# Performance work log

Hardware: AMD Instinct MI355X
Metric: run time of the kernel (lower is better)

Reference implementation:

```python
import jax, jax.numpy as jnp
import numpy as np

N_NODES = 50000
N_EDGES = 800000
HEADS = 2
HID = 64
NEG_SLOPE = 0.2


def setup_inputs() -> dict:
    key = jax.random.key(0)
    ks = jax.random.split(key, 8)
    x = jax.random.normal(ks[0], (N_NODES, 128), dtype=jnp.float32)
    W_src = jax.random.normal(ks[1], (128, HEADS * HID), dtype=jnp.float32) * (1.0 / np.sqrt(128))
    W_dst = jax.random.normal(ks[2], (128, HEADS * HID), dtype=jnp.float32) * (1.0 / np.sqrt(128))
    att_src = jax.random.normal(ks[3], (HEADS, HID), dtype=jnp.float32) * 0.1
    att_dst = jax.random.normal(ks[4], (HEADS, HID), dtype=jnp.float32) * 0.1
    bias = jax.random.normal(ks[5], (HEADS * HID,), dtype=jnp.float32) * 0.01
    prelu_w = jnp.full((HEADS * HID,), 0.25, dtype=jnp.float32)
    edge_index = jax.random.randint(ks[6], (2, N_EDGES), 0, N_NODES, dtype=jnp.int64)
    return {"x": x, "W_src": W_src, "W_dst": W_dst, "att_src": att_src,
            "att_dst": att_dst, "bias": bias, "prelu_w": prelu_w,
            "edge_index": edge_index}


def gat_prelu(x, W_src, W_dst, att_src, att_dst, bias, prelu_w, edge_index):
    N = x.shape[0]
    src, dst = edge_index[0], edge_index[1]
    xs = (x @ W_src).reshape(N, HEADS, HID)   # [N,H,C]
    xd = (x @ W_dst).reshape(N, HEADS, HID)
    a_src = jnp.einsum('nhc,hc->nh', xs, att_src)  # [N,H]
    a_dst = jnp.einsum('nhc,hc->nh', xd, att_dst)
    e = jax.nn.leaky_relu(a_src[src] + a_dst[dst], NEG_SLOPE)  # [E,H]
    # segment softmax over incoming edges of each dst node
    m = jax.ops.segment_max(e, dst, num_segments=N)            # [N,H]
    ee = jnp.exp(e - m[dst])
    denom = jax.ops.segment_sum(ee, dst, num_segments=N)
    alpha = ee / (denom[dst] + 1e-16)                          # [E,H]
    msg = xs[src] * alpha[:, :, None]                          # [E,H,C]
    out = jax.ops.segment_sum(msg, dst, num_segments=N)        # [N,H,C]
    out = out.reshape(N, HEADS * HID) + bias
    return jnp.where(out >= 0, out, prelu_w * out)


def reference(x, W_src, W_dst, att_src, att_dst, bias, prelu_w, edge_index):
    return gat_prelu(x, W_src, W_dst, att_src, att_dst, bias, prelu_w, edge_index)
```

## Files before the change

### kernel.cpp

```cpp
#include <hip/hip_runtime.h>
#include <hip/hip_fp16.h>


#define N_NODES 50000
#define N_EDGES 800000
#define CAP     56

#define OFF_A    0
#define OFF_CNT  800000
#define OFF_XS   1000000
#define OFF_BKT  13800000
#define OFF_SWZ  36200000

typedef _Float16 f16x8 __attribute__((ext_vector_type(8)));
typedef float    f32x4 __attribute__((ext_vector_type(4)));

__global__ __launch_bounds__(256) void k0_prep(
    const float* __restrict__ Wsrc, const float* __restrict__ Wdst,
    const float* __restrict__ att_s, const float* __restrict__ att_d,
    __half* __restrict__ swz, int* __restrict__ cnt)
{
    __shared__ float vS[128 * 4];
    const int nt = blockIdx.x;
    const int t = threadIdx.x;
    for (int i = nt * 256 + t; i < N_NODES; i += 9 * 256) cnt[i] = 0;

    if (nt == 8) {
        if (t < 128) {
            const float* wsp = Wsrc + t * 128;
            const float* wdp = Wdst + t * 128;
            float a0 = 0.f, a1 = 0.f, a2 = 0.f, a3 = 0.f;
#pragma unroll 8
            for (int c = 0; c < 64; ++c) {
                a0 += wsp[c]      * att_s[c];
                a1 += wsp[64 + c] * att_s[64 + c];
                a2 += wdp[c]      * att_d[c];
                a3 += wdp[64 + c] * att_d[64 + c];
            }
            *(float4*)(vS + t * 4) = make_float4(a0, a1, a2, a3);
        }
        __syncthreads();
    }
    const int kb = t >> 6, L = t & 63;
    const int col = L & 15;
    const int krow = kb * 32 + ((L >> 4) & 3) * 8;
    f16x8 v;
    if (nt < 8) {
#pragma unroll
        for (int j = 0; j < 8; ++j)
            v[j] = (_Float16)Wsrc[(size_t)(krow + j) * 128 + nt * 16 + col];
    } else {
#pragma unroll
        for (int j = 0; j < 8; ++j)
            v[j] = (col < 4) ? (_Float16)vS[(krow + j) * 4 + col] : (_Float16)0.f;
    }
    *(f16x8*)(swz + ((size_t)(kb * 9 + nt) * 64 + L) * 8) = v;
}

__global__ __launch_bounds__(256) void k1_gemm(
    const float* __restrict__ x, const __half* __restrict__ swz,
    __half* __restrict__ xs, float* __restrict__ a_all)
{
    const int t = threadIdx.x;
    const int w = t >> 6, L = t & 63;
    const int m = L & 15, q = L >> 4;
    const int n_a = blockIdx.x * 64 + w * 16 + m;
    const int rrow = (n_a < N_NODES) ? n_a : (N_NODES - 1);
    const float* xrow = x + (size_t)rrow * 128;

    f32x4 acc[9];
#pragma unroll
    for (int nt = 0; nt < 9; ++nt) acc[nt] = (f32x4){0.f, 0.f, 0.f, 0.f};

#pragma unroll
    for (int kb = 0; kb < 4; ++kb) {
        const int k0 = kb * 32 + q * 8;
        float4 xa = *(const float4*)(xrow + k0);
        float4 xb = *(const float4*)(xrow + k0 + 4);
        f16x8 a;
        a[0] = (_Float16)xa.x; a[1] = (_Float16)xa.y;
        a[2] = (_Float16)xa.z; a[3] = (_Float16)xa.w;
        a[4] = (_Float16)xb.x; a[5] = (_Float16)xb.y;
        a[6] = (_Float16)xb.z; a[7] = (_Float16)xb.w;
        const f16x8* bbase = (const f16x8*)swz + (size_t)(kb * 9) * 64 + L;
#pragma unroll
        for (int nt = 0; nt < 9; ++nt) {
            f16x8 b = bbase[(size_t)nt * 64];
            acc[nt] = __builtin_amdgcn_mfma_f32_16x16x32_f16(a, b, acc[nt], 0, 0, 0);
        }
    }

    const int rbase = blockIdx.x * 64 + w * 16 + q * 4;
#pragma unroll
    for (int nt = 0; nt < 8; ++nt) {
#pragma unroll
        for (int r = 0; r < 4; ++r) {
            int n = rbase + r;
            if (n < N_NODES)
                xs[(size_t)n * 128 + nt * 16 + m] = (__half)acc[nt][r];
        }
    }
    if (m < 4) {
#pragma unroll
        for (int r = 0; r < 4; ++r) {
            int n = rbase + r;
            if (n < N_NODES) a_all[(size_t)n * 4 + m] = acc[8][r];
        }
    }
}

__global__ __launch_bounds__(256) void k5_scatter(
    const int* __restrict__ ei, const float* __restrict__ a_all,
    int* __restrict__ cnt, int2* __restrict__ bkt)
{
    int e = (blockIdx.x * 256 + threadIdx.x) * 2;
    if (e >= N_EDGES) return;
    int2 ss = *(const int2*)(ei + e);
    int2 dd = *(const int2*)(ei + N_EDGES + e);
    float4 as0 = *(const float4*)(a_all + (size_t)ss.x * 4);
    float4 ad0 = *(const float4*)(a_all + (size_t)dd.x * 4);
    float4 as1 = *(const float4*)(a_all + (size_t)ss.y * 4);
    float4 ad1 = *(const float4*)(a_all + (size_t)dd.y * 4);

    float e00 = as0.x + ad0.z, e01 = as0.y + ad0.w;
    float e10 = as1.x + ad1.z, e11 = as1.y + ad1.w;
    e00 = (e00 >= 0.f) ? e00 : 0.2f * e00;
    e01 = (e01 >= 0.f) ? e01 : 0.2f * e01;
    e10 = (e10 >= 0.f) ? e10 : 0.2f * e10;
    e11 = (e11 >= 0.f) ? e11 : 0.2f * e11;
    __half2 hw0 = __floats2half2_rn(__expf(e00), __expf(e01));
    __half2 hw1 = __floats2half2_rn(__expf(e10), __expf(e11));

    int pos0 = atomicAdd(cnt + dd.x, 1);
    int pos1 = atomicAdd(cnt + dd.y, 1);
    if (pos0 < CAP) {
        int2 ent; ent.x = ss.x; ent.y = *reinterpret_cast<int*>(&hw0);
        bkt[(size_t)dd.x * CAP + pos0] = ent;
    }
    if (pos1 < CAP) {
        int2 ent; ent.x = ss.y; ent.y = *reinterpret_cast<int*>(&hw1);
        bkt[(size_t)dd.y * CAP + pos1] = ent;
    }
}

template<bool GUARD>
__device__ __forceinline__ void step8(const int2* __restrict__ row, int k, int m,
                                      int sh, int j, const __half* __restrict__ xs,
                                      float& ax, float& ay, float& sw)
{
    int4 p0 = *(const int4*)(row + k);
    int4 p1 = *(const int4*)(row + k + 2);
    int4 p2 = *(const int4*)(row + k + 4);
    int4 p3 = *(const int4*)(row + k + 6);
    int s0 = p0.x, s1 = p0.z, s2 = p1.x, s3 = p1.z;
    int s4 = p2.x, s5 = p2.z, s6 = p3.x, s7 = p3.z;
    unsigned w0 = (unsigned)p0.y, w1 = (unsigned)p0.w;
    unsigned w2 = (unsigned)p1.y, w3 = (unsigned)p1.w;
    unsigned w4 = (unsigned)p2.y, w5 = (unsigned)p2.w;
    unsigned w6 = (unsigned)p3.y, w7 = (unsigned)p3.w;
    if (GUARD) {
        if (k + 0 >= m) { s0 = 0; w0 = 0; }
        if (k + 1 >= m) { s1 = 0; w1 = 0; }
        if (k + 2 >= m) { s2 = 0; w2 = 0; }
        if (k + 3 >= m) { s3 = 0; w3 = 0; }
        if (k + 4 >= m) { s4 = 0; w4 = 0; }
        if (k + 5 >= m) { s5 = 0; w5 = 0; }
        if (k + 6 >= m) { s6 = 0; w6 = 0; }
        if (k + 7 >= m) { s7 = 0; w7 = 0; }
    }
    __half2 h0 = *(const __half2*)(xs + (size_t)s0 * 128 + j);
    __half2 h1 = *(const __half2*)(xs + (size_t)s1 * 128 + j);
    __half2 h2 = *(const __half2*)(xs + (size_t)s2 * 128 + j);
    __half2 h3 = *(const __half2*)(xs + (size_t)s3 * 128 + j);
    __half2 h4 = *(const __half2*)(xs + (size_t)s4 * 128 + j);
    __half2 h5 = *(const __half2*)(xs + (size_t)s5 * 128 + j);
    __half2 h6 = *(const __half2*)(xs + (size_t)s6 * 128 + j);
    __half2 h7 = *(const __half2*)(xs + (size_t)s7 * 128 + j);
    float a0 = __half2float(__ushort_as_half((unsigned short)(w0 >> sh)));
    float a1 = __half2float(__ushort_as_half((unsigned short)(w1 >> sh)));
    float a2 = __half2float(__ushort_as_half((unsigned short)(w2 >> sh)));
    float a3 = __half2float(__ushort_as_half((unsigned short)(w3 >> sh)));
    float a4 = __half2float(__ushort_as_half((unsigned short)(w4 >> sh)));
    float a5 = __half2float(__ushort_as_half((unsigned short)(w5 >> sh)));
    float a6 = __half2float(__ushort_as_half((unsigned short)(w6 >> sh)));
    float a7 = __half2float(__ushort_as_half((unsigned short)(w7 >> sh)));
    ax += __half2float(h0.x) * a0; ay += __half2float(h0.y) * a0;
    ax += __half2float(h1.x) * a1; ay += __half2float(h1.y) * a1;
    ax += __half2float(h2.x) * a2; ay += __half2float(h2.y) * a2;
    ax += __half2float(h3.x) * a3; ay += __half2float(h3.y) * a3;
    ax += __half2float(h4.x) * a4; ay += __half2float(h4.y) * a4;
    ax += __half2float(h5.x) * a5; ay += __half2float(h5.y) * a5;
    ax += __half2float(h6.x) * a6; ay += __half2float(h6.y) * a6;
    ax += __half2float(h7.x) * a7; ay += __half2float(h7.y) * a7;
    sw += ((a0 + a1) + (a2 + a3)) + ((a4 + a5) + (a6 + a7));
}

__global__ __launch_bounds__(256) void k6_agg(
    const int2* __restrict__ bkt, const int* __restrict__ cnt,
    const __half* __restrict__ xs, const float* __restrict__ bias,
    const float* __restrict__ prelu_w, float* __restrict__ out)
{
    const int n = blockIdx.x * 4 + (threadIdx.x >> 6);
    const int lane = threadIdx.x & 63;
    const int j = lane * 2;
    const int sh = (lane >> 5) * 16;
    int m = cnt[n]; if (m > CAP) m = CAP;
    const int2* row = bkt + (size_t)n * CAP;
    float ax = 0.f, ay = 0.f, sw = 0.f;
    int k = 0;
    for (; k + 8 <= m; k += 8)
        step8<false>(row, k, m, sh, j, xs, ax, ay, sw);
    if (k < m)
        step8<true>(row, k, m, sh, j, xs, ax, ay, sw);

    float inv = 1.f / (sw + 1e-16f);
    float o0 = ax * inv + bias[j];
    float o1 = ay * inv + bias[j + 1];
    float2 r;
    r.x = (o0 >= 0.f) ? o0 : prelu_w[j] * o0;
    r.y = (o1 >= 0.f) ? o1 : prelu_w[j + 1] * o1;
    *(float2*)(out + (size_t)n * 128 + j) = r;
}

extern "C" void kernel_launch(void* const* d_in, const int* in_sizes, int n_in,
                              void* d_out, int out_size, void* d_ws, size_t ws_size,
                              hipStream_t stream) {
    const float* x      = (const float*)d_in[0];
    const float* Wsrc   = (const float*)d_in[1];
    const float* Wdst   = (const float*)d_in[2];
    const float* att_s  = (const float*)d_in[3];
    const float* att_d  = (const float*)d_in[4];
    const float* bias   = (const float*)d_in[5];
    const float* prelu  = (const float*)d_in[6];
    const int*   ei     = (const int*)d_in[7];
    float* out = (float*)d_out;

    char* ws = (char*)d_ws;
    float*  a_all = (float*)(ws + OFF_A);
    int*    cnt   = (int*)(ws + OFF_CNT);
    __half* xs    = (__half*)(ws + OFF_XS);
    int2*   bkt   = (int2*)(ws + OFF_BKT);
    __half* swz   = (__half*)(ws + OFF_SWZ);

    k0_prep<<<9, 256, 0, stream>>>(Wsrc, Wdst, att_s, att_d, swz, cnt);
    k1_gemm<<<(N_NODES + 63) / 64, 256, 0, stream>>>(x, swz, xs, a_all);
    k5_scatter<<<(N_EDGES / 2 + 255) / 256, 256, 0, stream>>>(ei, a_all, cnt, bkt);
    k6_agg<<<N_NODES / 4, 256, 0, stream>>>(bkt, cnt, xs, bias, prelu, out);
}
```

Baseline: 193.8 us.

## Replace direct edge scatter with two-pass coarse/fine bucketed binning

Replaces the single scatter kernel, which did random global atomics and writes per edge, with two passes. First, edges are binned by the coarse destination range (1024 nodes) into per-block shared-memory rings and flushed in 8-entry chunks to coarse buckets, with the source and low destination bits packed into one 64-bit entry. Second, each coarse bucket is read sequentially and scattered into the per-node CAP buckets, so the atomics and writes land in a localized range. This adds a kernel launch and extra traffic, and uses the output buffer as scratch. Coarse buckets are capped at BCAP with no overflow handling, and the 16-bit source packing cannot hold indices of 65536 or more.

```diff
diff --git a/kernel.cpp b/kernel.cpp
--- a/kernel.cpp
+++ b/kernel.cpp
@@ -5,25 +5,31 @@
 #define N_NODES 50000
 #define N_EDGES 800000
 #define CAP     56
-
-#define OFF_A    0
-#define OFF_CNT  800000
-#define OFF_XS   1000000
-#define OFF_BKT  13800000
-#define OFF_SWZ  36200000
+#define NB      49
+#define BCAP    20480
+#define RING    64
+
+#define OFF_A      0
+#define OFF_CNT    800000
+#define OFF_GCUR   1000000
+#define OFF_XS     1000256
+#define OFF_BKT    13800256
+#define OFF_SWZ    36200256
 
 typedef _Float16 f16x8 __attribute__((ext_vector_type(8)));
 typedef float    f32x4 __attribute__((ext_vector_type(4)));
+typedef unsigned long long u64;
 
 __global__ __launch_bounds__(256) void k0_prep(
     const float* __restrict__ Wsrc, const float* __restrict__ Wdst,
     const float* __restrict__ att_s, const float* __restrict__ att_d,
-    __half* __restrict__ swz, int* __restrict__ cnt)
+    __half* __restrict__ swz, int* __restrict__ cnt, int* __restrict__ gcur)
 {
     __shared__ float vS[128 * 4];
     const int nt = blockIdx.x;
     const int t = threadIdx.x;
     for (int i = nt * 256 + t; i < N_NODES; i += 9 * 256) cnt[i] = 0;
+    if (nt == 0 && t < NB) gcur[t] = t * BCAP;
 
     if (nt == 8) {
         if (t < 128) {
@@ -109,37 +115,87 @@
     }
 }
 
-__global__ __launch_bounds__(256) void k5_scatter(
+__global__ __launch_bounds__(256) void kC_coarse(
     const int* __restrict__ ei, const float* __restrict__ a_all,
+    int* __restrict__ gcur, u64* __restrict__ coarse)
+{
+    __shared__ u64 ring[NB * RING];
+    __shared__ int lcnt[NB], ltail[NB];
+    const int t = threadIdx.x;
+    if (t < NB) { lcnt[t] = 0; ltail[t] = 0; }
+    __syncthreads();
+
+    const int per = gridDim.x * 512;
+    const int nIter = (N_EDGES + per - 1) / per;
+    for (int it = 0; it < nIter; ++it) {
+        const int base = it * per + blockIdx.x * 512;
+#pragma unroll
+        for (int u = 0; u < 2; ++u) {
+            int e = base + u * 256 + t;
+            if (e < N_EDGES) {
+                int s = ei[e];
+                int d = ei[N_EDGES + e];
+                float2 as = *(const float2*)(a_all + (size_t)s * 4);
+                float2 ad = *(const float2*)(a_all + (size_t)d * 4 + 2);
+                float e0 = as.x + ad.x;
+                float e1 = as.y + ad.y;
+                e0 = (e0 >= 0.f) ? e0 : 0.2f * e0;
+                e1 = (e1 >= 0.f) ? e1 : 0.2f * e1;
+                __half2 hw = __floats2half2_rn(__expf(e0), __expf(e1));
+                unsigned lo = (unsigned)s | ((unsigned)(d & 1023) << 16);
+                u64 ent = (u64)lo | ((u64)*reinterpret_cast<unsigned*>(&hw) << 32);
+                int b = d >> 10;
+                int pos = atomicAdd(&lcnt[b], 1);
+                ring[b * RING + (pos & (RING - 1))] = ent;
+            }
+        }
+        __syncthreads();
+        if (t < NB) {
+            int c = lcnt[t], tl = ltail[t];
+            while (c - tl >= 8) {
+                int gpos = atomicAdd(&gcur[t], 8);
+                if (gpos + 8 <= (t + 1) * BCAP) {
+                    u64* dst = coarse + gpos;
+#pragma unroll
+                    for (int i = 0; i < 8; ++i)
+                        dst[i] = ring[t * RING + ((tl + i) & (RING - 1))];
+                }
+                tl += 8;
+            }
+            ltail[t] = tl;
+        }
+        __syncthreads();
+    }
+    if (t < NB) {
+        int c = lcnt[t], tl = ltail[t], p = c - tl;
+        if (p > 0) {
+            int gpos = atomicAdd(&gcur[t], p);
+            if (gpos + p <= (t + 1) * BCAP)
+                for (int i = 0; i < p; ++i)
+                    coarse[gpos + i] = ring[t * RING + ((tl + i) & (RING - 1))];
+        }
+    }
+}
+
+__global__ __launch_bounds__(256) void kD_fine(
+    const u64* __restrict__ coarse, const int* __restrict__ gcur,
     int* __restrict__ cnt, int2* __restrict__ bkt)
 {
-    int e = (blockIdx.x * 256 + threadIdx.x) * 2;
-    if (e >= N_EDGES) return;
-    int2 ss = *(const int2*)(ei + e);
-    int2 dd = *(const int2*)(ei + N_EDGES + e);
-    float4 as0 = *(const float4*)(a_all + (size_t)ss.x * 4);
-    float4 ad0 = *(const float4*)(a_all + (size_t)dd.x * 4);
-    float4 as1 = *(const float4*)(a_all + (size_t)ss.y * 4);
-    float4 ad1 = *(const float4*)(a_all + (size_t)dd.y * 4);
-
-    float e00 = as0.x + ad0.z, e01 = as0.y + ad0.w;
-    float e10 = as1.x + ad1.z, e11 = as1.y + ad1.w;
-    e00 = (e00 >= 0.f) ? e00 : 0.2f * e00;
-    e01 = (e01 >= 0.f) ? e01 : 0.2f * e01;
-    e10 = (e10 >= 0.f) ? e10 : 0.2f * e10;
-    e11 = (e11 >= 0.f) ? e11 : 0.2f * e11;
-    __half2 hw0 = __floats2half2_rn(__expf(e00), __expf(e01));
-    __half2 hw1 = __floats2half2_rn(__expf(e10), __expf(e11));
-
-    int pos0 = atomicAdd(cnt + dd.x, 1);
-    int pos1 = atomicAdd(cnt + dd.y, 1);
-    if (pos0 < CAP) {
-        int2 ent; ent.x = ss.x; ent.y = *reinterpret_cast<int*>(&hw0);
-        bkt[(size_t)dd.x * CAP + pos0] = ent;
-    }
-    if (pos1 < CAP) {
-        int2 ent; ent.x = ss.y; ent.y = *reinterpret_cast<int*>(&hw1);
-        bkt[(size_t)dd.y * CAP + pos1] = ent;
+    const int b = blockIdx.x >> 3, qq = blockIdx.x & 7;
+    int cntb = gcur[b] - b * BCAP;
+    if (cntb > BCAP) cntb = BCAP;
+    const int per = (cntb + 7) >> 3;
+    const int lo = qq * per;
+    int hi = lo + per; if (hi > cntb) hi = cntb;
+    const u64* src = coarse + (size_t)b * BCAP;
+    for (int i = lo + threadIdx.x; i < hi; i += 256) {
+        u64 ent = src[i];
+        unsigned l = (unsigned)ent;
+        unsigned w = (unsigned)(ent >> 32);
+        int s = l & 0xFFFF;
+        int d = (b << 10) + ((l >> 16) & 1023);
+        int pos = atomicAdd(cnt + d, 1);
+        if (pos < CAP) bkt[(size_t)d * CAP + pos] = make_int2(s, (int)w);
     }
 }
 
@@ -236,14 +292,17 @@
     float* out = (float*)d_out;
 
     char* ws = (char*)d_ws;
-    float*  a_all = (float*)(ws + OFF_A);
-    int*    cnt   = (int*)(ws + OFF_CNT);
-    __half* xs    = (__half*)(ws + OFF_XS);
-    int2*   bkt   = (int2*)(ws + OFF_BKT);
-    __half* swz   = (__half*)(ws + OFF_SWZ);
-
-    k0_prep<<<9, 256, 0, stream>>>(Wsrc, Wdst, att_s, att_d, swz, cnt);
+    float*  a_all  = (float*)(ws + OFF_A);
+    int*    cnt    = (int*)(ws + OFF_CNT);
+    int*    gcur   = (int*)(ws + OFF_GCUR);
+    __half* xs     = (__half*)(ws + OFF_XS);
+    int2*   bkt    = (int2*)(ws + OFF_BKT);
+    __half* swz    = (__half*)(ws + OFF_SWZ);
+    u64*    coarse = (u64*)d_out;
+
+    k0_prep<<<9, 256, 0, stream>>>(Wsrc, Wdst, att_s, att_d, swz, cnt, gcur);
     k1_gemm<<<(N_NODES + 63) / 64, 256, 0, stream>>>(x, swz, xs, a_all);
-    k5_scatter<<<(N_EDGES / 2 + 255) / 256, 256, 0, stream>>>(ei, a_all, cnt, bkt);
+    kC_coarse<<<400, 256, 0, stream>>>(ei, a_all, gcur, coarse);
+    kD_fine<<<NB * 8, 256, 0, stream>>>(coarse, gcur, cnt, bkt);
     k6_agg<<<N_NODES / 4, 256, 0, stream>>>(bkt, cnt, xs, bias, prelu, out);
 }
```

After: 241.3 us. 24.5% more time.
